# Optimization experiments

Measured on AMD Instinct MI355X. Metric: run time of the kernel, lower is better.

Reference implementation:

```python
import jax, jax.numpy as jnp
import numpy as np

B, C, H, W = 8, 256, 32, 32
DK, HEADS = 64, 4
DQ = DK * HEADS            # lambda attention: query dim = dim_key * num_heads
DV = 256 // HEADS          # out_channels // num_heads
EPS = 1e-5
SF = DK ** (-0.25)


def setup_inputs() -> dict:
    key = jax.random.key(0)
    ks = jax.random.split(key, 6)
    inv = 1.0 / np.sqrt(C)
    return {
        "input": jax.random.normal(ks[0], (B, C, H, W), jnp.float32),
        "Wq": jax.random.normal(ks[1], (DQ, C), jnp.float32) * inv,
        "gamma_q": jnp.ones((DQ,), jnp.float32),
        "beta_q": jnp.zeros((DQ,), jnp.float32),
        "Wk": jax.random.normal(ks[2], (DK, C), jnp.float32) * inv,
        "gamma_k": jnp.ones((DK,), jnp.float32),
        "beta_k": jnp.zeros((DK,), jnp.float32),
        "Wv": jax.random.normal(ks[3], (DV, C), jnp.float32) * inv,
        "rpe": jax.random.normal(ks[4], (2 * max(H, W) - 1, 2 * max(H, W) - 1, DK), jnp.float32),
    }


def _bn(x, gamma, beta):
    # BatchNorm2d in training mode: batch stats over (B, H, W), biased variance
    mu = jnp.mean(x, axis=(0, 2, 3), keepdims=True)
    var = jnp.var(x, axis=(0, 2, 3), keepdims=True)
    xn = (x - mu) * jax.lax.rsqrt(var + EPS)
    return xn * gamma[None, :, None, None] + beta[None, :, None, None]


def reference(input, Wq, gamma_q, beta_q, Wk, gamma_k, beta_k, Wv, rpe):
    b, c, h, w = input.shape
    n = h * w
    size = max(h, w)

    # conv1x1 projections (no bias)
    q = _bn(jnp.einsum('oc,bchw->bohw', Wq, input), gamma_q, beta_q)
    k = _bn(jnp.einsum('oc,bchw->bohw', Wk, input), gamma_k, beta_k)
    v = jnp.einsum('oc,bchw->bohw', Wv, input)

    q = q.reshape(b, HEADS, DK, n) * SF          # [b,h,k,n]
    k = k.reshape(b, DK, n) * SF                 # single kv head -> [b,k,n]
    v = v.reshape(b, DV, n)                      # [b,v,n]

    # lambda attention: content lambda
    ks = jax.nn.softmax(k, axis=-1)
    context = jnp.einsum('bkn,bvn->bkv', ks, v)
    out = jnp.einsum('bkv,bhkn->bhvn', context, q)

    # positional lambda via relative position embedding gather
    pos = jnp.arange(size)
    grid = jnp.stack(jnp.meshgrid(pos, pos, indexing='ij'), axis=-1).reshape(-1, 2)  # [n,2]
    rel = grid[None, :] - grid[:, None] + (size - 1)                                 # [n,n,2]
    rg = rpe[rel[..., 0], rel[..., 1]]                                               # [n,n,k]
    pos_context = jnp.einsum('nmk,bvm->bnkv', rg, v)
    out = out + jnp.einsum('bhkn,bnkv->bhvn', q, pos_context)

    return out.reshape(b, -1, h, w)
```

## Files before the change

### kernel.cpp

```cpp
#include <hip/hip_runtime.h>

#define SFC 0.35355339059327373f

typedef __attribute__((ext_vector_type(8))) short short8;
typedef __attribute__((ext_vector_type(16))) float f32x16;
typedef unsigned short ushort_t;

__device__ __forceinline__ float4 ld4(const float* p) { return *reinterpret_cast<const float4*>(p); }
__device__ __forceinline__ void st4(float* p, float4 v) { *reinterpret_cast<float4*>(p) = v; }

union F4 { float4 v; float f[4]; };
union S8 { short8 v; ushort_t u[8]; };

__device__ __forceinline__ ushort_t bfb(float f) {
  union { float f; unsigned u; } a; a.f = f;
  unsigned r = a.u + 0x7FFFu + ((a.u >> 16) & 1u);
  return (ushort_t)(r >> 16);
}
__device__ __forceinline__ float bf2f(ushort_t u) {
  union { unsigned u; float f; } a; a.u = (unsigned)u << 16; return a.f;
}

__device__ __forceinline__ void gl16(const void* g, void* l) {
  __builtin_amdgcn_global_load_lds(
      (const __attribute__((address_space(1))) unsigned int*)g,
      (__attribute__((address_space(3))) unsigned int*)l, 16, 0, 0);
}

__global__ __launch_bounds__(256) void k_prep(
    const float* __restrict__ rpe, const float* __restrict__ wq,
    const float* __restrict__ wk, const float* __restrict__ wv,
    const float* __restrict__ x, ushort_t* __restrict__ RPEB2,
    ushort_t* __restrict__ WB, ushort_t* __restrict__ XBT)
{
  const int bx = blockIdx.x, t = threadIdx.x;
  if (bx < 63) {
    const int di = bx;
#pragma unroll
    for (int it = 0; it < 2; ++it) {
      const int slot = t + it * 256;
      const int tkc = slot >> 6;
      const int l = slot & 63, lnp = l & 31, hip = l >> 5;
      const int dj = (tkc >> 2) * 32 + lnp;
      const int k = (tkc & 3) * 16 + hip * 8;
      S8 o;
      if (dj < 63) {
        const float* s = rpe + (size_t)di * 4032 + dj * 64 + k;
        float4 a = ld4(s), b = ld4(s + 4);
        o.u[0] = bfb(a.x); o.u[1] = bfb(a.y); o.u[2] = bfb(a.z); o.u[3] = bfb(a.w);
        o.u[4] = bfb(b.x); o.u[5] = bfb(b.y); o.u[6] = bfb(b.z); o.u[7] = bfb(b.w);
      } else {
#pragma unroll
        for (int i = 0; i < 8; ++i) o.u[i] = 0;
      }
      *(short8*)(RPEB2 + (size_t)di * 4096 + tkc * 512 + l * 8) = o.v;
    }
  } else if (bx < 111) {
    const int cc = (bx - 63) * 256 + t;
    const int o = cc >> 5, k8 = (cc & 31) * 8;
    const float* src = (o < 256) ? (wq + o * 256)
                      : (o < 320) ? (wk + (o - 256) * 256)
                                  : (wv + (o - 320) * 256);
    float4 a = ld4(src + k8), b = ld4(src + k8 + 4);
    S8 s;
    s.u[0] = bfb(a.x); s.u[1] = bfb(a.y); s.u[2] = bfb(a.z); s.u[3] = bfb(a.w);
    s.u[4] = bfb(b.x); s.u[5] = bfb(b.y); s.u[6] = bfb(b.z); s.u[7] = bfb(b.w);
    *(short8*)(WB + (size_t)o * 256 + k8) = s.v;
  } else {
    const int id = (bx - 111) * 256 + t;
    const int ng = id & 8191, c8 = id >> 13;
    const int bb = ng >> 10, nn = ng & 1023;
    const float* src = x + (size_t)bb * 262144 + (size_t)(c8 * 8) * 1024 + nn;
    S8 s;
#pragma unroll
    for (int j = 0; j < 8; ++j) s.u[j] = bfb(src[(size_t)j * 1024]);
    *(short8*)(XBT + (size_t)ng * 256 + c8 * 8) = s.v;
  }
}

__global__ __launch_bounds__(256) void k_projm(
    const ushort_t* __restrict__ WB, const ushort_t* __restrict__ XBT,
    float* __restrict__ Pk, ushort_t* __restrict__ QB,
    ushort_t* __restrict__ VB2, float* __restrict__ PSUM,
    float* __restrict__ PSQ)
{
  __shared__ ushort_t SM[13824];
  ushort_t* At = SM;
  ushort_t* Bt = SM + 4608;
  const int t = threadIdx.x;
  const int bm = blockIdx.x, bn = blockIdx.y;
  const int o0 = bm * 64, col0 = bn * 128;
  const int w = t >> 6, l = t & 63, ln = l & 31, hi = l >> 5;
  const int wm = w & 1, wn = w >> 1;

  f32x16 acc0, acc1;
#pragma unroll
  for (int i = 0; i < 16; ++i) { acc0[i] = 0.f; acc1[i] = 0.f; }

  for (int k0 = 0; k0 < 256; k0 += 64) {
    __syncthreads();
#pragma unroll
    for (int i = 0; i < 2; ++i) {
      const int c = t + i * 256, row = c >> 3, k8 = (c & 7) * 8;
      *(short8*)(At + row * 72 + k8) =
          *(const short8*)(WB + (size_t)(o0 + row) * 256 + k0 + k8);
    }
#pragma unroll
    for (int i = 0; i < 4; ++i) {
      const int c = t + i * 256, row = c >> 3, k8 = (c & 7) * 8;
      *(short8*)(Bt + row * 72 + k8) =
          *(const short8*)(XBT + (size_t)(col0 + row) * 256 + k0 + k8);
    }
    __syncthreads();
    const ushort_t* ka  = At + (wm * 32 + ln) * 72 + hi * 8;
    const ushort_t* kb0 = Bt + (wn * 64 + ln) * 72 + hi * 8;
    const ushort_t* kb1 = Bt + (wn * 64 + 32 + ln) * 72 + hi * 8;
#pragma unroll
    for (int kc = 0; kc < 4; ++kc) {
      short8 a = *(const short8*)(ka + kc * 16);
      acc0 = __builtin_amdgcn_mfma_f32_32x32x16_bf16(a, *(const short8*)(kb0 + kc * 16), acc0, 0, 0, 0);
      acc1 = __builtin_amdgcn_mfma_f32_32x32x16_bf16(a, *(const short8*)(kb1 + kc * 16), acc1, 0, 0, 0);
    }
  }

  if (bm == 5) {
    __syncthreads();
    {
      const int n0l = wn * 64 + ln;
#pragma unroll
      for (int r = 0; r < 16; ++r) {
        const int v = wm * 32 + (r & 3) + 8 * (r >> 2) + 4 * hi;
#pragma unroll
        for (int half = 0; half < 2; ++half) {
          const int nl = n0l + half * 32;
          const int i2l = nl >> 5, j2 = nl & 31;
          const float val = half ? acc1[r] : acc0[r];
          SM[((i2l * 4 + wm * 2 + (j2 >> 4)) << 9)
             + ((v & 31) + 32 * ((j2 >> 3) & 1)) * 8 + (j2 & 7)] = bfb(val);
        }
      }
    }
    __syncthreads();
    {
      const int b2 = bn >> 3, i2b0 = (bn & 7) * 4;
      const int slot = t >> 4, off = (t & 15) * 32;
      const int i2l = slot >> 2, sub = slot & 3;
      ushort_t* gdst = VB2 + ((size_t)((b2 * 32 + i2b0 + i2l) * 4 + sub)) * 512 + off;
      const ushort_t* lsrc = SM + slot * 512 + off;
#pragma unroll
      for (int c = 0; c < 4; ++c)
        *(short8*)(gdst + c * 8) = *(const short8*)(lsrc + c * 8);
    }
  } else if (bm == 4) {
#pragma unroll
    for (int r = 0; r < 16; ++r) {
      const int o = o0 + wm * 32 + (r & 3) + 8 * (r >> 2) + 4 * hi;
      float* dst = Pk + (size_t)(o - 256) * 8192 + col0 + wn * 64 + ln;
      dst[0]  = acc0[r];
      dst[32] = acc1[r];
    }
#pragma unroll
    for (int r = 0; r < 16; ++r) {
      float s1 = acc0[r] + acc1[r];
      float s2 = acc0[r] * acc0[r] + acc1[r] * acc1[r];
#pragma unroll
      for (int off = 1; off < 32; off <<= 1) {
        s1 += __shfl_xor(s1, off, 64);
        s2 += __shfl_xor(s2, off, 64);
      }
      if (ln == 0) {
        const int o = o0 + wm * 32 + (r & 3) + 8 * (r >> 2) + 4 * hi;
        PSUM[o * 128 + bn * 2 + wn] = s1;
        PSQ [o * 128 + bn * 2 + wn] = s2;
      }
    }
  } else {
#pragma unroll
    for (int r = 0; r < 16; ++r) {
      float s1 = acc0[r] + acc1[r];
      float s2 = acc0[r] * acc0[r] + acc1[r] * acc1[r];
#pragma unroll
      for (int off = 1; off < 32; off <<= 1) {
        s1 += __shfl_xor(s1, off, 64);
        s2 += __shfl_xor(s2, off, 64);
      }
      if (ln == 0) {
        const int o = o0 + wm * 32 + (r & 3) + 8 * (r >> 2) + 4 * hi;
        PSUM[o * 128 + bn * 2 + wn] = s1;
        PSQ [o * 128 + bn * 2 + wn] = s2;
      }
    }
    __syncthreads();
    {
      const int kcq = 2 * wm;
#pragma unroll
      for (int r = 0; r < 16; ++r) {
        const int kc = kcq + ((r >> 3) & 1);
        const int lq = ln + 32 * ((r >> 2) & 1);
        const int iq = (r & 3) + 4 * hi;
#pragma unroll
        for (int half = 0; half < 2; ++half) {
          const int i1l = wn * 2 + half;
          const float val = half ? acc1[r] : acc0[r];
          SM[((i1l * 4 + kc) << 9) + lq * 8 + iq] = bfb(val);
        }
      }
    }
    __syncthreads();
    {
      const int b0 = col0 >> 10, i1b = (col0 >> 5) & 31;
      const int slot = t >> 4, off = (t & 15) * 32;
      const int i1l = slot >> 2, kc2 = slot & 3;
      ushort_t* gdst = QB + (((size_t)(b0 * 32 + i1b + i1l) * 4 + bm) * 4 + kc2) * 512 + off;
      const ushort_t* lsrc = SM + slot * 512 + off;
#pragma unroll
      for (int c = 0; c < 4; ++c)
        *(short8*)(gdst + c * 8) = *(const short8*)(lsrc + c * 8);
    }
  }
}

__global__ __launch_bounds__(256) void k_softctx(
    const float* __restrict__ Pk, const float* __restrict__ PSUM,
    const float* __restrict__ PSQ, const float* __restrict__ gq,
    const float* __restrict__ bq, const float* __restrict__ gk,
    const float* __restrict__ bk, float* __restrict__ SCALE,
    float* __restrict__ SHIFT, const ushort_t* __restrict__ VB2,
    ushort_t* __restrict__ CTXB)
{
  __shared__ float red[8];
  __shared__ float scsh[2];
  __shared__ float cpart[4][64];
  const int t = threadIdx.x;

  if (blockIdx.x >= 512) {
    const int ch = blockIdx.x - 512;
    float s1 = 0.f, s2 = 0.f;
    if (t < 128) { s1 = PSUM[ch * 128 + t]; s2 = PSQ[ch * 128 + t]; }
#pragma unroll
    for (int off = 1; off < 64; off <<= 1) {
      s1 += __shfl_xor(s1, off, 64);
      s2 += __shfl_xor(s2, off, 64);
    }
    if ((t & 63) == 0) { red[t >> 6] = s1; red[4 + (t >> 6)] = s2; }
    __syncthreads();
    if (t == 0) {
      s1 = red[0] + red[1] + red[2] + red[3];
      s2 = red[4] + red[5] + red[6] + red[7];
      const float mu = s1 * (1.0f / 8192.0f);
      const float var = s2 * (1.0f / 8192.0f) - mu * mu;
      const float sc = rsqrtf(var + 1e-5f) * gq[ch] * SFC;
      SCALE[ch] = sc;
      SHIFT[ch] = bq[ch] * SFC - mu * sc;
    }
    return;
  }

  const int b = blockIdx.x >> 6, kc = blockIdx.x & 63;
  {
    const int ch = 256 + kc;
    float s1 = 0.f, s2 = 0.f;
    if (t < 128) { s1 = PSUM[ch * 128 + t]; s2 = PSQ[ch * 128 + t]; }
#pragma unroll
    for (int off = 1; off < 64; off <<= 1) {
      s1 += __shfl_xor(s1, off, 64);
      s2 += __shfl_xor(s2, off, 64);
    }
    if ((t & 63) == 0) { red[t >> 6] = s1; red[4 + (t >> 6)] = s2; }
    __syncthreads();
    if (t == 0) {
      s1 = red[0] + red[1] + red[2] + red[3];
      s2 = red[4] + red[5] + red[6] + red[7];
      const float mu = s1 * (1.0f / 8192.0f);
      const float var = s2 * (1.0f / 8192.0f) - mu * mu;
      const float sc = rsqrtf(var + 1e-5f) * gk[kc] * SFC;
      scsh[0] = sc;
      scsh[1] = bk[kc] * SFC - mu * sc;
    }
    __syncthreads();
  }
  const float sc = scsh[0], sh = scsh[1];

  const float4* rowp = (const float4*)(Pk + (size_t)kc * 8192 + b * 1024);
  float4 pv = rowp[t];
  float y0 = pv.x * sc + sh, y1 = pv.y * sc + sh;
  float y2 = pv.z * sc + sh, y3 = pv.w * sc + sh;
  float m = fmaxf(fmaxf(y0, y1), fmaxf(y2, y3));
#pragma unroll
  for (int off = 32; off; off >>= 1) m = fmaxf(m, __shfl_xor(m, off, 64));
  __shared__ float red2[8];
  const int w = t >> 6, l = t & 63;
  if (l == 0) red2[w] = m;
  __syncthreads();
  m = fmaxf(fmaxf(red2[0], red2[1]), fmaxf(red2[2], red2[3]));
  const float e0 = __expf(y0 - m), e1 = __expf(y1 - m);
  const float e2 = __expf(y2 - m), e3 = __expf(y3 - m);
  float su = e0 + e1 + e2 + e3;
#pragma unroll
  for (int off = 32; off; off >>= 1) su += __shfl_xor(su, off, 64);
  if (l == 0) red2[4 + w] = su;
  __syncthreads();
  const float inv = 1.0f / (red2[4] + red2[5] + red2[6] + red2[7]);
  const float k0v = e0 * inv, k1v = e1 * inv, k2v = e2 * inv, k3v = e3 * inv;

  const int n0 = t * 4;
  const int i2 = n0 >> 5;
  const int cX = (n0 >> 4) & 1, hi2 = (n0 >> 3) & 1, i0 = n0 & 7;
  const ushort_t* vbL = VB2 + (((size_t)(b * 32 + i2) * 2 + 0) * 2 + cX) * 512
                        + (32 * hi2) * 8 + i0;
  const ushort_t* vbH = vbL + 1024;
  float a64[64];
#pragma unroll
  for (int v = 0; v < 32; ++v) {
    ushort4 u = *(const ushort4*)(vbL + v * 8);
    a64[v] = k0v * bf2f(u.x) + k1v * bf2f(u.y) + k2v * bf2f(u.z) + k3v * bf2f(u.w);
  }
#pragma unroll
  for (int v = 0; v < 32; ++v) {
    ushort4 u = *(const ushort4*)(vbH + v * 8);
    a64[32 + v] = k0v * bf2f(u.x) + k1v * bf2f(u.y) + k2v * bf2f(u.z) + k3v * bf2f(u.w);
  }
  float c32[32];
#pragma unroll
  for (int j = 0; j < 32; ++j) {
    const float mine = (l & 32) ? a64[j + 32] : a64[j];
    const float send = (l & 32) ? a64[j] : a64[j + 32];
    c32[j] = mine + __shfl_xor(send, 32, 64);
  }
  float c16[16];
#pragma unroll
  for (int j = 0; j < 16; ++j) {
    const float mine = (l & 16) ? c32[j + 16] : c32[j];
    const float send = (l & 16) ? c32[j] : c32[j + 16];
    c16[j] = mine + __shfl_xor(send, 16, 64);
  }
  float c8[8];
#pragma unroll
  for (int j = 0; j < 8; ++j) {
    const float mine = (l & 8) ? c16[j + 8] : c16[j];
    const float send = (l & 8) ? c16[j] : c16[j + 8];
    c8[j] = mine + __shfl_xor(send, 8, 64);
  }
  float c4[4];
#pragma unroll
  for (int j = 0; j < 4; ++j) {
    const float mine = (l & 4) ? c8[j + 4] : c8[j];
    const float send = (l & 4) ? c8[j] : c8[j + 4];
    c4[j] = mine + __shfl_xor(send, 4, 64);
  }
  float c2[2];
#pragma unroll
  for (int j = 0; j < 2; ++j) {
    const float mine = (l & 2) ? c4[j + 2] : c4[j];
    const float send = (l & 2) ? c4[j] : c4[j + 2];
    c2[j] = mine + __shfl_xor(send, 2, 64);
  }
  {
    const float mine = (l & 1) ? c2[1] : c2[0];
    const float send = (l & 1) ? c2[0] : c2[1];
    cpart[w][l] = mine + __shfl_xor(send, 1, 64);
  }
  __syncthreads();
  if (w == 0) {
    const float s = cpart[0][l] + cpart[1][l] + cpart[2][l] + cpart[3][l];
    CTXB[(size_t)b * 4608 + l * 72 + kc] = bfb(s);
  }
}

extern __shared__ char ldsc[];

__global__ __launch_bounds__(512, 4) void k_pos(
    const ushort_t* __restrict__ QB, const ushort_t* __restrict__ RPEB2,
    const ushort_t* __restrict__ VB2, const float* __restrict__ SCALE,
    const float* __restrict__ SHIFT, const ushort_t* __restrict__ CTXB,
    float* __restrict__ out)
{
  float* out_l = (float*)ldsc;
  ushort_t* SlB = (ushort_t*)(ldsc + 33792);
  char* CtxL = ldsc + 54272;

  const int t = threadIdx.x;
  const int b = blockIdx.x >> 5, i1 = blockIdx.x & 31;
  const int w = t >> 6, l = t & 63, ln = l & 31, hi = l >> 5;
  const int m = w & 3, g = w >> 2;

  {
    const char* cs = (const char*)CTXB + (size_t)b * 9216;
    gl16(cs + w * 1024 + l * 16, CtxL + w * 1024 + l * 16);
    if (w == 0) gl16(cs + 8192 + l * 16, CtxL + 8192 + l * 16);
  }

  const ushort_t* rbase = RPEB2 + (size_t)(g * 16 - i1 + 31) * 4096;
  const ushort_t* vbase = VB2 + (size_t)(b * 32 + g * 16) * 2048;

  short8 rA[8];
#pragma unroll
  for (int f = 0; f < 8; ++f) rA[f] = *(const short8*)(rbase + f * 512 + l * 8);

  short8 qf[4];
  {
    const ushort_t* qb = QB + (((size_t)(b * 32 + i1) * 4 + m) * 4) * 512 + l * 8;
#pragma unroll
    for (int kc = 0; kc < 4; ++kc) {
      S8 raw; raw.v = *(const short8*)(qb + kc * 512);
      const int chb = m * 64 + kc * 16 + hi * 8;
      F4 s0, s1, h0, h1;
      s0.v = ld4(SCALE + chb); s1.v = ld4(SCALE + chb + 4);
      h0.v = ld4(SHIFT + chb); h1.v = ld4(SHIFT + chb + 4);
      S8 o;
#pragma unroll
      for (int i = 0; i < 8; ++i) {
        const float f = bf2f(raw.u[i]);
        const float scv = (i < 4) ? s0.f[i] : s1.f[i - 4];
        const float shv = (i < 4) ? h0.f[i] : h1.f[i - 4];
        o.u[i] = bfb(f * scv + shv);
      }
      qf[kc] = o.v;
    }
  }

  f32x16 sv0, sv1;
#pragma unroll
  for (int i = 0; i < 16; ++i) { sv0[i] = 0.f; sv1[i] = 0.f; }

  ushort_t* sm = SlB + w * 1280;

  for (int s = 0; s < 16; ++s) {
    f32x16 t0, t1;
#pragma unroll
    for (int i = 0; i < 16; ++i) { t0[i] = 0.f; t1[i] = 0.f; }
#pragma unroll
    for (int kc = 0; kc < 4; ++kc) {
      t0 = __builtin_amdgcn_mfma_f32_32x32x16_bf16(qf[kc], rA[kc],     t0, 0, 0, 0);
      t1 = __builtin_amdgcn_mfma_f32_32x32x16_bf16(qf[kc], rA[4 + kc], t1, 0, 0, 0);
    }
    if (s + 1 < 16) {
      const ushort_t* rn = rbase + (size_t)(s + 1) * 4096;
#pragma unroll
      for (int f = 0; f < 8; ++f) rA[f] = *(const short8*)(rn + f * 512 + l * 8);
    }
#pragma unroll
    for (int r = 0; r < 16; ++r) {
      const int j1 = (r & 3) + 8 * (r >> 2) + 4 * hi;
      const int j2a = ln + j1 - 31;
      const bool useA = (j2a >= 0);
      const int j2 = useA ? j2a : (j2a + 32);
      sm[j1 * 40 + j2] = bfb(useA ? t0[r] : t1[r]);
    }
    const ushort_t* sa = sm + ln * 40 + hi * 8;
    short8 sA0 = *(const short8*)(sa);
    short8 sA1 = *(const short8*)(sa + 16);
    const ushort_t* vp = vbase + (size_t)s * 2048 + l * 8;
    {
      short8 v00 = *(const short8*)(vp);
      short8 v01 = *(const short8*)(vp + 512);
      sv0 = __builtin_amdgcn_mfma_f32_32x32x16_bf16(sA0, v00, sv0, 0, 0, 0);
      sv0 = __builtin_amdgcn_mfma_f32_32x32x16_bf16(sA1, v01, sv0, 0, 0, 0);
    }
    {
      short8 v10 = *(const short8*)(vp + 1024);
      short8 v11 = *(const short8*)(vp + 1536);
      sv1 = __builtin_amdgcn_mfma_f32_32x32x16_bf16(sA0, v10, sv1, 0, 0, 0);
      sv1 = __builtin_amdgcn_mfma_f32_32x32x16_bf16(sA1, v11, sv1, 0, 0, 0);
    }
  }

  __syncthreads();

  if (g == 0) {
    const ushort_t* cb = (const ushort_t*)CtxL;
    const ushort_t* c0 = cb + ln * 72 + hi * 8;
    const ushort_t* c1 = cb + (32 + ln) * 72 + hi * 8;
#pragma unroll
    for (int kc = 0; kc < 4; ++kc) {
      sv0 = __builtin_amdgcn_mfma_f32_32x32x16_bf16(qf[kc], *(const short8*)(c0 + kc * 16), sv0, 0, 0, 0);
      sv1 = __builtin_amdgcn_mfma_f32_32x32x16_bf16(qf[kc], *(const short8*)(c1 + kc * 16), sv1, 0, 0, 0);
    }
  } else {
#pragma unroll
    for (int r = 0; r < 16; ++r) {
      const int j1 = (r & 3) + 8 * (r >> 2) + 4 * hi;
      out_l[(m * 64 + ln) * 33 + j1]      = sv0[r];
      out_l[(m * 64 + 32 + ln) * 33 + j1] = sv1[r];
    }
  }
  __syncthreads();
  if (g == 0) {
#pragma unroll
    for (int r = 0; r < 16; ++r) {
      const int j1 = (r & 3) + 8 * (r >> 2) + 4 * hi;
      out_l[(m * 64 + ln) * 33 + j1]      += sv0[r];
      out_l[(m * 64 + 32 + ln) * 33 + j1] += sv1[r];
    }
  }
  __syncthreads();
  {
    const int ch = t >> 1, jh = (t & 1) * 16;
    float* dst = out + (size_t)b * 262144 + (size_t)ch * 1024 + i1 * 32 + jh;
    const float* srow = out_l + ch * 33 + jh;
#pragma unroll
    for (int gq2 = 0; gq2 < 4; ++gq2)
      st4(dst + gq2 * 4, make_float4(srow[gq2 * 4], srow[gq2 * 4 + 1],
                                     srow[gq2 * 4 + 2], srow[gq2 * 4 + 3]));
  }
}

extern "C" void kernel_launch(void* const* d_in, const int* in_sizes, int n_in,
                              void* d_out, int out_size, void* d_ws, size_t ws_size,
                              hipStream_t stream) {
  const float* x   = (const float*)d_in[0];
  const float* wq  = (const float*)d_in[1];
  const float* gq  = (const float*)d_in[2];
  const float* bq  = (const float*)d_in[3];
  const float* wk  = (const float*)d_in[4];
  const float* gk  = (const float*)d_in[5];
  const float* bk  = (const float*)d_in[6];
  const float* wv  = (const float*)d_in[7];
  const float* rpe = (const float*)d_in[8];
  float* out = (float*)d_out;
  char* W = (char*)d_ws;

  float* Pk       = (float*)W;
  ushort_t* QB    = (ushort_t*)(W + 2097152);
  float* PSUM     = (float*)(W + 6291456);
  float* PSQ      = (float*)(W + 6455296);
  float* SCALE    = (float*)(W + 6619136);
  float* SHIFT    = (float*)(W + 6621184);
  ushort_t* CTXB  = (ushort_t*)(W + 6623232);
  ushort_t* RPEB2 = (ushort_t*)(W + 6696960);
  ushort_t* VB2   = (ushort_t*)(W + 7213056);
  ushort_t* WB    = (ushort_t*)(W + 8261632);
  ushort_t* XBT   = (ushort_t*)(W + 8458240);

  k_prep<<<1135, 256, 0, stream>>>(rpe, wq, wk, wv, x, RPEB2, WB, XBT);
  k_projm<<<dim3(6, 64), 256, 0, stream>>>(WB, XBT, Pk, QB, VB2, PSUM, PSQ);
  k_softctx<<<768, 256, 0, stream>>>(Pk, PSUM, PSQ, gq, bq, gk, bk,
                                     SCALE, SHIFT, VB2, CTXB);

  hipFuncSetAttribute((const void*)k_pos,
                      hipFuncAttributeMaxDynamicSharedMemorySize, 63488);
  k_pos<<<256, 512, 63488, stream>>>(QB, RPEB2, VB2, SCALE, SHIFT, CTXB, out);
}
```

Before: 57.11 us.

## Fuse bf16 conversion prep kernel into projection GEMM and softmax-context kernels

Removes the separate k_prep launch. The projection GEMM now reads fp32 weights and input directly, converting them to bf16 while staging tiles into shared memory, with the input transposed on the fly. The rpe-to-bf16 repacking moves into the spare BN-stats blocks of k_softctx. This drops a kernel launch and the workspace round-trip for the converted weights and input. In exchange, weight and input tiles are re-read and re-converted by every block that uses them, and the input loads are strided scalar reads.

```diff
diff --git a/kernel.cpp b/kernel.cpp
--- a/kernel.cpp
+++ b/kernel.cpp
@@ -27,72 +27,26 @@
       (__attribute__((address_space(3))) unsigned int*)l, 16, 0, 0);
 }
 
-__global__ __launch_bounds__(256) void k_prep(
-    const float* __restrict__ rpe, const float* __restrict__ wq,
-    const float* __restrict__ wk, const float* __restrict__ wv,
-    const float* __restrict__ x, ushort_t* __restrict__ RPEB2,
-    ushort_t* __restrict__ WB, ushort_t* __restrict__ XBT)
-{
-  const int bx = blockIdx.x, t = threadIdx.x;
-  if (bx < 63) {
-    const int di = bx;
-#pragma unroll
-    for (int it = 0; it < 2; ++it) {
-      const int slot = t + it * 256;
-      const int tkc = slot >> 6;
-      const int l = slot & 63, lnp = l & 31, hip = l >> 5;
-      const int dj = (tkc >> 2) * 32 + lnp;
-      const int k = (tkc & 3) * 16 + hip * 8;
-      S8 o;
-      if (dj < 63) {
-        const float* s = rpe + (size_t)di * 4032 + dj * 64 + k;
-        float4 a = ld4(s), b = ld4(s + 4);
-        o.u[0] = bfb(a.x); o.u[1] = bfb(a.y); o.u[2] = bfb(a.z); o.u[3] = bfb(a.w);
-        o.u[4] = bfb(b.x); o.u[5] = bfb(b.y); o.u[6] = bfb(b.z); o.u[7] = bfb(b.w);
-      } else {
-#pragma unroll
-        for (int i = 0; i < 8; ++i) o.u[i] = 0;
-      }
-      *(short8*)(RPEB2 + (size_t)di * 4096 + tkc * 512 + l * 8) = o.v;
-    }
-  } else if (bx < 111) {
-    const int cc = (bx - 63) * 256 + t;
-    const int o = cc >> 5, k8 = (cc & 31) * 8;
-    const float* src = (o < 256) ? (wq + o * 256)
-                      : (o < 320) ? (wk + (o - 256) * 256)
-                                  : (wv + (o - 320) * 256);
-    float4 a = ld4(src + k8), b = ld4(src + k8 + 4);
-    S8 s;
-    s.u[0] = bfb(a.x); s.u[1] = bfb(a.y); s.u[2] = bfb(a.z); s.u[3] = bfb(a.w);
-    s.u[4] = bfb(b.x); s.u[5] = bfb(b.y); s.u[6] = bfb(b.z); s.u[7] = bfb(b.w);
-    *(short8*)(WB + (size_t)o * 256 + k8) = s.v;
-  } else {
-    const int id = (bx - 111) * 256 + t;
-    const int ng = id & 8191, c8 = id >> 13;
-    const int bb = ng >> 10, nn = ng & 1023;
-    const float* src = x + (size_t)bb * 262144 + (size_t)(c8 * 8) * 1024 + nn;
-    S8 s;
-#pragma unroll
-    for (int j = 0; j < 8; ++j) s.u[j] = bfb(src[(size_t)j * 1024]);
-    *(short8*)(XBT + (size_t)ng * 256 + c8 * 8) = s.v;
-  }
-}
-
 __global__ __launch_bounds__(256) void k_projm(
-    const ushort_t* __restrict__ WB, const ushort_t* __restrict__ XBT,
+    const float* __restrict__ wq, const float* __restrict__ wk,
+    const float* __restrict__ wv, const float* __restrict__ x,
     float* __restrict__ Pk, ushort_t* __restrict__ QB,
     ushort_t* __restrict__ VB2, float* __restrict__ PSUM,
     float* __restrict__ PSQ)
 {
-  __shared__ ushort_t SM[13824];
+  __shared__ ushort_t SM[14848];
   ushort_t* At = SM;
   ushort_t* Bt = SM + 4608;
   const int t = threadIdx.x;
   const int bm = blockIdx.x, bn = blockIdx.y;
   const int o0 = bm * 64, col0 = bn * 128;
+  const int b_img = bn >> 3, n0 = (bn & 7) * 128;
   const int w = t >> 6, l = t & 63, ln = l & 31, hi = l >> 5;
   const int wm = w & 1, wn = w >> 1;
 
+  const float* wsrc = (bm < 4) ? (wq + (size_t)o0 * 256)
+                    : (bm == 4) ? wk : wv;
+
   f32x16 acc0, acc1;
 #pragma unroll
   for (int i = 0; i < 16; ++i) { acc0[i] = 0.f; acc1[i] = 0.f; }
@@ -102,19 +56,30 @@
 #pragma unroll
     for (int i = 0; i < 2; ++i) {
       const int c = t + i * 256, row = c >> 3, k8 = (c & 7) * 8;
-      *(short8*)(At + row * 72 + k8) =
-          *(const short8*)(WB + (size_t)(o0 + row) * 256 + k0 + k8);
-    }
-#pragma unroll
-    for (int i = 0; i < 4; ++i) {
-      const int c = t + i * 256, row = c >> 3, k8 = (c & 7) * 8;
-      *(short8*)(Bt + row * 72 + k8) =
-          *(const short8*)(XBT + (size_t)(col0 + row) * 256 + k0 + k8);
+      const float* wr = wsrc + (size_t)row * 256 + k0 + k8;
+      float4 a = ld4(wr), b2 = ld4(wr + 4);
+      S8 s;
+      s.u[0] = bfb(a.x); s.u[1] = bfb(a.y); s.u[2] = bfb(a.z); s.u[3] = bfb(a.w);
+      s.u[4] = bfb(b2.x); s.u[5] = bfb(b2.y); s.u[6] = bfb(b2.z); s.u[7] = bfb(b2.w);
+      *(short8*)(At + row * 72 + k8) = s.v;
+    }
+    {
+      const int nn = t & 31, cg = t >> 5;
+      const float* xc = x + (size_t)b_img * 262144
+                        + (size_t)(k0 + cg * 8) * 1024 + n0 + nn;
+#pragma unroll
+      for (int jj = 0; jj < 4; ++jj) {
+        S8 s;
+#pragma unroll
+        for (int ci = 0; ci < 8; ++ci)
+          s.u[ci] = bfb(xc[(size_t)ci * 1024 + 32 * jj]);
+        *(short8*)(Bt + (nn + 32 * jj) * 80 + cg * 8) = s.v;
+      }
     }
     __syncthreads();
     const ushort_t* ka  = At + (wm * 32 + ln) * 72 + hi * 8;
-    const ushort_t* kb0 = Bt + (wn * 64 + ln) * 72 + hi * 8;
-    const ushort_t* kb1 = Bt + (wn * 64 + 32 + ln) * 72 + hi * 8;
+    const ushort_t* kb0 = Bt + (wn * 64 + ln) * 80 + hi * 8;
+    const ushort_t* kb1 = Bt + (wn * 64 + 32 + ln) * 80 + hi * 8;
 #pragma unroll
     for (int kc = 0; kc < 4; ++kc) {
       short8 a = *(const short8*)(ka + kc * 16);
@@ -224,8 +189,9 @@
     const float* __restrict__ Pk, const float* __restrict__ PSUM,
     const float* __restrict__ PSQ, const float* __restrict__ gq,
     const float* __restrict__ bq, const float* __restrict__ gk,
-    const float* __restrict__ bk, float* __restrict__ SCALE,
-    float* __restrict__ SHIFT, const ushort_t* __restrict__ VB2,
+    const float* __restrict__ bk, const float* __restrict__ rpe,
+    float* __restrict__ SCALE, float* __restrict__ SHIFT,
+    const ushort_t* __restrict__ VB2, ushort_t* __restrict__ RPEB2,
     ushort_t* __restrict__ CTXB)
 {
   __shared__ float red[8];
@@ -234,7 +200,28 @@
   const int t = threadIdx.x;
 
   if (blockIdx.x >= 512) {
-    const int ch = blockIdx.x - 512;
+    const int virt = blockIdx.x - 512;
+    {
+      const int slot = virt * 256 + t;
+      if (slot < 32256) {
+        const int di = slot >> 9, s2 = slot & 511;
+        const int tkc = s2 >> 6, l2 = s2 & 63, lnp = l2 & 31, hip = l2 >> 5;
+        const int dj = (tkc >> 2) * 32 + lnp;
+        const int k = (tkc & 3) * 16 + hip * 8;
+        S8 o;
+        if (dj < 63) {
+          const float* s = rpe + (size_t)di * 4032 + dj * 64 + k;
+          float4 a = ld4(s), b2 = ld4(s + 4);
+          o.u[0] = bfb(a.x); o.u[1] = bfb(a.y); o.u[2] = bfb(a.z); o.u[3] = bfb(a.w);
+          o.u[4] = bfb(b2.x); o.u[5] = bfb(b2.y); o.u[6] = bfb(b2.z); o.u[7] = bfb(b2.w);
+        } else {
+#pragma unroll
+          for (int i = 0; i < 8; ++i) o.u[i] = 0;
+        }
+        *(short8*)(RPEB2 + (size_t)di * 4096 + tkc * 512 + l2 * 8) = o.v;
+      }
+    }
+    const int ch = virt;
     float s1 = 0.f, s2 = 0.f;
     if (t < 128) { s1 = PSUM[ch * 128 + t]; s2 = PSQ[ch * 128 + t]; }
 #pragma unroll
@@ -529,13 +516,10 @@
   ushort_t* CTXB  = (ushort_t*)(W + 6623232);
   ushort_t* RPEB2 = (ushort_t*)(W + 6696960);
   ushort_t* VB2   = (ushort_t*)(W + 7213056);
-  ushort_t* WB    = (ushort_t*)(W + 8261632);
-  ushort_t* XBT   = (ushort_t*)(W + 8458240);
-
-  k_prep<<<1135, 256, 0, stream>>>(rpe, wq, wk, wv, x, RPEB2, WB, XBT);
-  k_projm<<<dim3(6, 64), 256, 0, stream>>>(WB, XBT, Pk, QB, VB2, PSUM, PSQ);
-  k_softctx<<<768, 256, 0, stream>>>(Pk, PSUM, PSQ, gq, bq, gk, bk,
-                                     SCALE, SHIFT, VB2, CTXB);
+
+  k_projm<<<dim3(6, 64), 256, 0, stream>>>(wq, wk, wv, x, Pk, QB, VB2, PSUM, PSQ);
+  k_softctx<<<768, 256, 0, stream>>>(Pk, PSUM, PSQ, gq, bq, gk, bk, rpe,
+                                     SCALE, SHIFT, VB2, RPEB2, CTXB);
 
   hipFuncSetAttribute((const void*)k_pos,
                       hipFuncAttributeMaxDynamicSharedMemorySize, 63488);
```

Measured after the change: 58.64 us. 2.7% more time.

## Split k_pos blocks across head pairs with four-way row-group reduction

Applied to the files above, without the earlier changes.

Each k_pos block now handles two of the four heads instead of all four, doubling the grid to 512 blocks. Within a block the eight waves are split as two heads times four row groups of 8 rows each, replacing two row groups of 16. The partial results are reduced serially through LDS in four barrier-separated stages. The aim is to fill more CUs and shorten each wave's serial loop over rows. In exchange, each block loads Q and the RPE tiles redundantly and the reduction needs more synchronization steps.

```diff
diff --git a/kernel.cpp b/kernel.cpp
--- a/kernel.cpp
+++ b/kernel.cpp
@@ -376,13 +376,16 @@
     float* __restrict__ out)
 {
   float* out_l = (float*)ldsc;
-  ushort_t* SlB = (ushort_t*)(ldsc + 33792);
-  char* CtxL = ldsc + 54272;
+  ushort_t* SlB = (ushort_t*)(ldsc + 16896);
+  char* CtxL = ldsc + 37376;
 
   const int t = threadIdx.x;
-  const int b = blockIdx.x >> 5, i1 = blockIdx.x & 31;
+  const int b = blockIdx.x >> 6;
+  const int i1 = (blockIdx.x >> 1) & 31;
+  const int hp = blockIdx.x & 1;
   const int w = t >> 6, l = t & 63, ln = l & 31, hi = l >> 5;
-  const int m = w & 3, g = w >> 2;
+  const int h2 = w & 1, g = w >> 1;
+  const int m = hp * 2 + h2;
 
   {
     const char* cs = (const char*)CTXB + (size_t)b * 9216;
@@ -390,8 +393,8 @@
     if (w == 0) gl16(cs + 8192 + l * 16, CtxL + 8192 + l * 16);
   }
 
-  const ushort_t* rbase = RPEB2 + (size_t)(g * 16 - i1 + 31) * 4096;
-  const ushort_t* vbase = VB2 + (size_t)(b * 32 + g * 16) * 2048;
+  const ushort_t* rbase = RPEB2 + (size_t)(g * 8 - i1 + 31) * 4096;
+  const ushort_t* vbase = VB2 + (size_t)(b * 32 + g * 8) * 2048;
 
   short8 rA[8];
 #pragma unroll
@@ -425,7 +428,7 @@
 
   ushort_t* sm = SlB + w * 1280;
 
-  for (int s = 0; s < 16; ++s) {
+  for (int s = 0; s < 8; ++s) {
     f32x16 t0, t1;
 #pragma unroll
     for (int i = 0; i < 16; ++i) { t0[i] = 0.f; t1[i] = 0.f; }
@@ -434,7 +437,7 @@
       t0 = __builtin_amdgcn_mfma_f32_32x32x16_bf16(qf[kc], rA[kc],     t0, 0, 0, 0);
       t1 = __builtin_amdgcn_mfma_f32_32x32x16_bf16(qf[kc], rA[4 + kc], t1, 0, 0, 0);
     }
-    if (s + 1 < 16) {
+    if (s + 1 < 8) {
       const ushort_t* rn = rbase + (size_t)(s + 1) * 4096;
 #pragma unroll
       for (int f = 0; f < 8; ++f) rA[f] = *(const short8*)(rn + f * 512 + l * 8);
@@ -476,32 +479,34 @@
       sv0 = __builtin_amdgcn_mfma_f32_32x32x16_bf16(qf[kc], *(const short8*)(c0 + kc * 16), sv0, 0, 0, 0);
       sv1 = __builtin_amdgcn_mfma_f32_32x32x16_bf16(qf[kc], *(const short8*)(c1 + kc * 16), sv1, 0, 0, 0);
     }
-  } else {
+  }
+
+  auto emit = [&](bool add) {
 #pragma unroll
     for (int r = 0; r < 16; ++r) {
       const int j1 = (r & 3) + 8 * (r >> 2) + 4 * hi;
-      out_l[(m * 64 + ln) * 33 + j1]      = sv0[r];
-      out_l[(m * 64 + 32 + ln) * 33 + j1] = sv1[r];
-    }
-  }
-  __syncthreads();
-  if (g == 0) {
-#pragma unroll
-    for (int r = 0; r < 16; ++r) {
-      const int j1 = (r & 3) + 8 * (r >> 2) + 4 * hi;
-      out_l[(m * 64 + ln) * 33 + j1]      += sv0[r];
-      out_l[(m * 64 + 32 + ln) * 33 + j1] += sv1[r];
-    }
-  }
-  __syncthreads();
+      float* p0 = &out_l[(h2 * 64 + ln) * 33 + j1];
+      float* p1 = &out_l[(h2 * 64 + 32 + ln) * 33 + j1];
+      if (add) { *p0 += sv0[r]; *p1 += sv1[r]; }
+      else     { *p0 = sv0[r];  *p1 = sv1[r]; }
+    }
+  };
+  if (g == 3) emit(false);
+  __syncthreads();
+  if (g == 2) emit(true);
+  __syncthreads();
+  if (g == 1) emit(true);
+  __syncthreads();
+  if (g == 0) emit(true);
+  __syncthreads();
+
   {
-    const int ch = t >> 1, jh = (t & 1) * 16;
-    float* dst = out + (size_t)b * 262144 + (size_t)ch * 1024 + i1 * 32 + jh;
+    const int ch = t >> 2, jh = (t & 3) * 8;
+    float* dst = out + (size_t)b * 262144 + (size_t)(hp * 128 + ch) * 1024
+                 + i1 * 32 + jh;
     const float* srow = out_l + ch * 33 + jh;
-#pragma unroll
-    for (int gq2 = 0; gq2 < 4; ++gq2)
-      st4(dst + gq2 * 4, make_float4(srow[gq2 * 4], srow[gq2 * 4 + 1],
-                                     srow[gq2 * 4 + 2], srow[gq2 * 4 + 3]));
+    st4(dst,     make_float4(srow[0], srow[1], srow[2], srow[3]));
+    st4(dst + 4, make_float4(srow[4], srow[5], srow[6], srow[7]));
   }
 }
 
@@ -538,6 +543,6 @@
                                      SCALE, SHIFT, VB2, CTXB);
 
   hipFuncSetAttribute((const void*)k_pos,
-                      hipFuncAttributeMaxDynamicSharedMemorySize, 63488);
-  k_pos<<<256, 512, 63488, stream>>>(QB, RPEB2, VB2, SCALE, SHIFT, CTXB, out);
-}
+                      hipFuncAttributeMaxDynamicSharedMemorySize, 46592);
+  k_pos<<<512, 512, 46592, stream>>>(QB, RPEB2, VB2, SCALE, SHIFT, CTXB, out);
+}
```

Result: no change. 56.73 us (median of 2 runs) (-0.7%).
